# Kernel tuning notes

Measured on AMD Instinct MI355X. Metric: run time of the kernel, lower is better.

The kernel has to match this reference:

```python
import jax, jax.numpy as jnp
import numpy as np

H = 180  # hidden size
T = 240  # timesteps

def lstm_cell_zero_state(x, Wih, bih, bhh):
    # torch nn.LSTMCell called with no (h, c): h = c = 0, so the W_hh term
    # vanishes and f-gate * c_prev vanishes. Gate order in torch: i, f, g, o.
    # x: [B, T, F] -> vectorized over all timesteps at once (no recurrence).
    gates = jnp.einsum('btf,gf->btg', x, Wih) + bih + bhh  # [B, T, 4H]
    i, f, g, o = jnp.split(gates, 4, axis=-1)
    c = jax.nn.sigmoid(i) * jnp.tanh(g)
    h = jax.nn.sigmoid(o) * jnp.tanh(c)
    return h  # [B, T, H]

def setup_inputs() -> dict:
    key = jax.random.key(0)
    ks = jax.random.split(key, 8)
    B = 2048
    s = lambda fan_in: 1.0 / np.sqrt(fan_in)
    x = jax.random.normal(ks[0], (B, 3, 60, T), dtype=jnp.float32)
    # Encoder LSTMCell(180 -> 180)
    W_ih_enc = jax.random.uniform(ks[1], (4 * H, 180), jnp.float32, -s(H), s(H))
    b_ih_enc = jax.random.uniform(ks[2], (4 * H,), jnp.float32, -s(H), s(H))
    b_hh_enc = jax.random.uniform(ks[3], (4 * H,), jnp.float32, -s(H), s(H))
    # Decoder LSTMCell(180 -> 180)
    W_ih_dec = jax.random.uniform(ks[4], (4 * H, H), jnp.float32, -s(H), s(H))
    b_ih_dec = jax.random.uniform(ks[5], (4 * H,), jnp.float32, -s(H), s(H))
    b_hh_dec = jax.random.uniform(ks[6], (4 * H,), jnp.float32, -s(H), s(H))
    # Output Linear(240*180 -> 40)
    W_out = jax.random.uniform(ks[7], (40, T * H), jnp.float32, -s(T * H), s(T * H))
    b_out = jnp.zeros((40,), jnp.float32)
    return {"x": x, "W_ih_enc": W_ih_enc, "b_ih_enc": b_ih_enc, "b_hh_enc": b_hh_enc,
            "W_ih_dec": W_ih_dec, "b_ih_dec": b_ih_dec, "b_hh_dec": b_hh_dec,
            "W_out": W_out, "b_out": b_out}

def reference(x, W_ih_enc, b_ih_enc, b_hh_enc, W_ih_dec, b_ih_dec, b_hh_dec, W_out, b_out):
    B = x.shape[0]
    # Encoder: [B,3,60,240] -> [B,240,3,60] -> [B,240,180]
    xe = jnp.transpose(x, (0, 3, 1, 2)).reshape(B, T, 3 * 60)
    h_enc = lstm_cell_zero_state(xe, W_ih_enc, b_ih_enc, b_hh_enc)  # [B,T,H]
    enc = jax.nn.softmax(h_enc, axis=2)
    # Decoder LSTM (also zero-state every step)
    h_dec = lstm_cell_zero_state(enc, W_ih_dec, b_ih_dec, b_hh_dec)  # [B,T,H]
    flat = h_dec.reshape(B, T * H)
    logits = flat @ W_out.T + b_out  # [B,40]
    out = jax.nn.softmax(logits.reshape(B, 4, 10), axis=2)
    return out
```

## Files before the change

### kernel.cpp

```cpp
#include <hip/hip_runtime.h>
#include <hip/hip_bf16.h>

#define HH 180
#define TT 240
#define KP 192
#define MP 576
#define LSTR 194
#define KOUT 43200
#define BB 2048

typedef __attribute__((ext_vector_type(8))) short short8;
typedef __attribute__((ext_vector_type(4))) float float4v;

__device__ inline unsigned short f2bf(float f) {
    unsigned u = __builtin_bit_cast(unsigned, f);
    u += 0x7fffu + ((u >> 16) & 1u);
    return (unsigned short)(u >> 16);
}
__device__ inline float bf2f(unsigned short h) {
    unsigned u = ((unsigned)h) << 16;
    return __builtin_bit_cast(float, u);
}
__device__ inline float sigm(float x) {
    return __builtin_amdgcn_rcpf(1.f + __expf(-x));
}
__device__ inline float tanh_(float x) {
    return 2.f * __builtin_amdgcn_rcpf(1.f + __expf(-2.f * x)) - 1.f;
}

__global__ void prep_kernel(const float* __restrict__ W1, const float* __restrict__ bi1,
                            const float* __restrict__ bh1, const float* __restrict__ W2,
                            const float* __restrict__ bi2, const float* __restrict__ bh2,
                            const float* __restrict__ Wo,
                            unsigned short* __restrict__ W1p, unsigned short* __restrict__ W2p,
                            float* __restrict__ bEp, float* __restrict__ bDp,
                            unsigned short* __restrict__ Wop, float* __restrict__ logits)
{
    int id = blockIdx.x * 256 + threadIdx.x;
    if (id < MP * KP) {
        int mp = id / KP, k = id % KP;
        int g = mp / KP, h = mp % KP;
        unsigned short v1 = 0, v2 = 0;
        if (h < HH && k < HH) {
            int r = (g == 0) ? h : (g == 1 ? 360 + h : 540 + h);
            v1 = f2bf(W1[r * HH + k]);
            v2 = f2bf(W2[r * HH + k]);
        }
        W1p[id] = v1; W2p[id] = v2;
    }
    if (id < MP) {
        int g = id / KP, h = id % KP;
        float v1 = 0.f, v2 = 0.f;
        if (h < HH) {
            int r = (g == 0) ? h : (g == 1 ? 360 + h : 540 + h);
            v1 = bi1[r] + bh1[r];
            v2 = bi2[r] + bh2[r];
        }
        bEp[id] = v1; bDp[id] = v2;
    }
    if (id < 48 * KOUT) {
        int n = id / KOUT, k = id % KOUT;
        Wop[id] = (n < 40) ? f2bf(Wo[n * KOUT + k]) : (unsigned short)0;
    }
    if (id < BB * 40) logits[id] = 0.f;
}

__global__ __launch_bounds__(256, 2) void phaseA_kernel(
    const float* __restrict__ x, const unsigned short* __restrict__ W1p,
    const unsigned short* __restrict__ W2p, const float* __restrict__ bEp,
    const float* __restrict__ bDp, unsigned short* __restrict__ hdec)
{
    __shared__ __align__(16) unsigned short Xs[128 * LSTR];
    __shared__ float bEs[MP], bDs[MP], sred[256];

    const int tid = threadIdx.x;
    const int b = blockIdx.x >> 1;
    const int t0 = (blockIdx.x & 1) * 112;
    const float* xb = x + (size_t)b * HH * TT;

    for (int i = tid; i < MP; i += 256) { bEs[i] = bEp[i]; bDs[i] = bDp[i]; }

    {
        const int c = tid & 127, half = tid >> 7;
        unsigned* lu = (unsigned*)Xs;
        const int cbase = c * (LSTR / 2);
        for (int i = 0; i < 45; ++i) {
            int f = half * 90 + 2 * i;
            float a0 = xb[f * TT + t0 + c];
            float a1 = xb[(f + 1) * TT + t0 + c];
            lu[cbase + (f >> 1)] = (unsigned)f2bf(a0) | ((unsigned)f2bf(a1) << 16);
        }
        if (half == 0) {
            for (int j = 0; j < 7; ++j) lu[cbase + 90 + j] = 0u;
        }
    }
    __syncthreads();

    const int lane = tid & 63, wv = tid >> 6;
    const int ch = wv >> 1, par = wv & 1;
    const int l15 = lane & 15, l4 = lane >> 4;

    short8 Bf[4][6];
    {
        const unsigned* lu = (const unsigned*)Xs;
        for (int nt = 0; nt < 4; ++nt) {
            int col = ch * 64 + nt * 16 + l15;
            int base = col * (LSTR / 2) + l4 * 4;
            #pragma unroll
            for (int ks = 0; ks < 6; ++ks) {
                union { unsigned u[4]; short8 v; } t;
                int idx = base + ks * 16;
                t.u[0] = lu[idx]; t.u[1] = lu[idx + 1];
                t.u[2] = lu[idx + 2]; t.u[3] = lu[idx + 3];
                Bf[nt][ks] = t.v;
            }
        }
    }
    __syncthreads();

    {
        const uint4* W1q = (const uint4*)W1p;
        for (int tri = par; tri < 12; tri += 2) {
            float4v acc[3][4];
            #pragma unroll
            for (int s = 0; s < 3; ++s)
                #pragma unroll
                for (int n = 0; n < 4; ++n) acc[s][n] = (float4v){0.f, 0.f, 0.f, 0.f};
            #pragma unroll
            for (int sec = 0; sec < 3; ++sec) {
                int abase = (sec * KP + tri * 16 + l15) * (KP / 8) + l4;
                #pragma unroll
                for (int ks = 0; ks < 6; ++ks) {
                    union { uint4 q; short8 v; } a;
                    a.q = W1q[abase + ks * 4];
                    #pragma unroll
                    for (int nt = 0; nt < 4; ++nt)
                        acc[sec][nt] = __builtin_amdgcn_mfma_f32_16x16x32_bf16(
                            a.v, Bf[nt][ks], acc[sec][nt], 0, 0, 0);
                }
            }
            unsigned* lw = (unsigned*)Xs;
            const int h0 = tri * 16 + l4 * 4;
            #pragma unroll
            for (int nt = 0; nt < 4; ++nt) {
                int col = ch * 64 + nt * 16 + l15;
                unsigned pk[2];
                #pragma unroll
                for (int e = 0; e < 4; ++e) {
                    int h = h0 + e;
                    float gi = acc[0][nt][e] + bEs[h];
                    float gg = acc[1][nt][e] + bEs[KP + h];
                    float go = acc[2][nt][e] + bEs[2 * KP + h];
                    float cc = sigm(gi) * tanh_(gg);
                    float hv = sigm(go) * tanh_(cc);
                    ((unsigned short*)pk)[e] = f2bf(__expf(hv));
                }
                lw[col * (LSTR / 2) + (h0 >> 1)] = pk[0];
                lw[col * (LSTR / 2) + (h0 >> 1) + 1] = pk[1];
            }
        }
    }
    __syncthreads();

    {
        const int c = tid & 127, half = tid >> 7;
        const unsigned* lu = (const unsigned*)Xs;
        int base = c * (LSTR / 2) + half * 45;
        float s = 0.f;
        for (int j = 0; j < 45; ++j) {
            unsigned u = lu[base + j];
            s += bf2f((unsigned short)u) + bf2f((unsigned short)(u >> 16));
        }
        sred[half * 128 + c] = s;
    }
    __syncthreads();

    {
        const unsigned* lu = (const unsigned*)Xs;
        for (int nt = 0; nt < 4; ++nt) {
            int col = ch * 64 + nt * 16 + l15;
            int base = col * (LSTR / 2) + l4 * 4;
            #pragma unroll
            for (int ks = 0; ks < 6; ++ks) {
                union { unsigned u[4]; short8 v; } t;
                int idx = base + ks * 16;
                t.u[0] = lu[idx]; t.u[1] = lu[idx + 1];
                t.u[2] = lu[idx + 2]; t.u[3] = lu[idx + 3];
                Bf[nt][ks] = t.v;
            }
        }
    }
    float rs[4];
    #pragma unroll
    for (int nt = 0; nt < 4; ++nt) {
        int col = ch * 64 + nt * 16 + l15;
        rs[nt] = __builtin_amdgcn_rcpf(sred[col] + sred[128 + col]);
    }

    {
        const uint4* W2q = (const uint4*)W2p;
        unsigned short* hout = hdec + (size_t)b * TT * HH;
        for (int tri = par; tri < 12; tri += 2) {
            float4v acc[3][4];
            #pragma unroll
            for (int s = 0; s < 3; ++s)
                #pragma unroll
                for (int n = 0; n < 4; ++n) acc[s][n] = (float4v){0.f, 0.f, 0.f, 0.f};
            #pragma unroll
            for (int sec = 0; sec < 3; ++sec) {
                int abase = (sec * KP + tri * 16 + l15) * (KP / 8) + l4;
                #pragma unroll
                for (int ks = 0; ks < 6; ++ks) {
                    union { uint4 q; short8 v; } a;
                    a.q = W2q[abase + ks * 4];
                    #pragma unroll
                    for (int nt = 0; nt < 4; ++nt)
                        acc[sec][nt] = __builtin_amdgcn_mfma_f32_16x16x32_bf16(
                            a.v, Bf[nt][ks], acc[sec][nt], 0, 0, 0);
                }
            }
            const int h0 = tri * 16 + l4 * 4;
            if (h0 < HH) {
                #pragma unroll
                for (int nt = 0; nt < 4; ++nt) {
                    int col = ch * 64 + nt * 16 + l15;
                    unsigned pk[2];
                    #pragma unroll
                    for (int e = 0; e < 4; ++e) {
                        int h = h0 + e;
                        float gi = acc[0][nt][e] * rs[nt] + bDs[h];
                        float gg = acc[1][nt][e] * rs[nt] + bDs[KP + h];
                        float go = acc[2][nt][e] * rs[nt] + bDs[2 * KP + h];
                        float cc = sigm(gi) * tanh_(gg);
                        float hv = sigm(go) * tanh_(cc);
                        ((unsigned short*)pk)[e] = f2bf(hv);
                    }
                    uint2 pv; pv.x = pk[0]; pv.y = pk[1];
                    *(uint2*)(hout + (size_t)(t0 + col) * HH + h0) = pv;
                }
            }
        }
    }
}

__global__ __launch_bounds__(256, 4) void phaseB_kernel(
    const unsigned short* __restrict__ hdec, const unsigned short* __restrict__ Wop,
    float* __restrict__ logits)
{
    const int tid = threadIdx.x;
    const int lane = tid & 63, wv = tid >> 6;
    const int l15 = lane & 15, l4 = lane >> 4;
    const int m0 = blockIdx.x * 64 + wv * 16;
    const int k0 = blockIdx.y * 1440;

    const uint4* Aq = (const uint4*)hdec;
    const uint4* Bq = (const uint4*)Wop;
    const int QK = KOUT / 8;
    int abase = (m0 + l15) * QK + (k0 >> 3) + l4;
    int bbase = l15 * QK + (k0 >> 3) + l4;

    float4v acc[3];
    #pragma unroll
    for (int n = 0; n < 3; ++n) acc[n] = (float4v){0.f, 0.f, 0.f, 0.f};

    #pragma unroll 3
    for (int ks = 0; ks < 45; ++ks) {
        union { uint4 q; short8 v; } a, b0, b1, b2;
        a.q  = Aq[abase + ks * 4];
        b0.q = Bq[bbase + ks * 4];
        b1.q = Bq[bbase + 16 * QK + ks * 4];
        b2.q = Bq[bbase + 32 * QK + ks * 4];
        acc[0] = __builtin_amdgcn_mfma_f32_16x16x32_bf16(a.v, b0.v, acc[0], 0, 0, 0);
        acc[1] = __builtin_amdgcn_mfma_f32_16x16x32_bf16(a.v, b1.v, acc[1], 0, 0, 0);
        acc[2] = __builtin_amdgcn_mfma_f32_16x16x32_bf16(a.v, b2.v, acc[2], 0, 0, 0);
    }

    #pragma unroll
    for (int nt = 0; nt < 3; ++nt) {
        int o = nt * 16 + l15;
        if (o < 40) {
            #pragma unroll
            for (int e = 0; e < 4; ++e) {
                int row = m0 + l4 * 4 + e;
                atomicAdd(&logits[row * 40 + o], acc[nt][e]);
            }
        }
    }
}

__global__ void out_kernel(const float* __restrict__ logits, const float* __restrict__ bout,
                           float* __restrict__ out)
{
    int id = blockIdx.x * 256 + threadIdx.x;
    if (id >= BB * 4) return;
    int b = id >> 2, j = id & 3;
    float v[10], mx = -1e30f;
    #pragma unroll
    for (int d = 0; d < 10; ++d) {
        v[d] = logits[b * 40 + j * 10 + d] + bout[j * 10 + d];
        mx = fmaxf(mx, v[d]);
    }
    float s = 0.f;
    #pragma unroll
    for (int d = 0; d < 10; ++d) { v[d] = __expf(v[d] - mx); s += v[d]; }
    float r = __builtin_amdgcn_rcpf(s);
    #pragma unroll
    for (int d = 0; d < 10; ++d) out[b * 40 + j * 10 + d] = v[d] * r;
}

extern "C" void kernel_launch(void* const* d_in, const int* in_sizes, int n_in,
                              void* d_out, int out_size, void* d_ws, size_t ws_size,
                              hipStream_t stream)
{
    const float* x    = (const float*)d_in[0];
    const float* W1   = (const float*)d_in[1];
    const float* bi1  = (const float*)d_in[2];
    const float* bh1  = (const float*)d_in[3];
    const float* W2   = (const float*)d_in[4];
    const float* bi2  = (const float*)d_in[5];
    const float* bh2  = (const float*)d_in[6];
    const float* Wo   = (const float*)d_in[7];
    const float* bout = (const float*)d_in[8];

    char* ws = (char*)d_ws;
    unsigned short* W1p = (unsigned short*)(ws + 0);
    unsigned short* W2p = (unsigned short*)(ws + 221184);
    float* bEp          = (float*)(ws + 442368);
    float* bDp          = (float*)(ws + 444928);
    unsigned short* Wop = (unsigned short*)(ws + 447488);
    float* logits       = (float*)(ws + 4594688);
    unsigned short* hdec= (unsigned short*)(ws + 4922368);

    prep_kernel<<<(48 * KOUT + 255) / 256, 256, 0, stream>>>(
        W1, bi1, bh1, W2, bi2, bh2, Wo, W1p, W2p, bEp, bDp, Wop, logits);
    phaseA_kernel<<<BB * 2, 256, 0, stream>>>(x, W1p, W2p, bEp, bDp, hdec);
    phaseB_kernel<<<dim3(32, 30), 256, 0, stream>>>(hdec, Wop, logits);
    out_kernel<<<(BB * 4 + 255) / 256, 256, 0, stream>>>(logits, bout, (float*)d_out);
}
```

Measured before the change: 1.058 ms.

## Split phaseA into four 60-column blocks per batch to raise occupancy

Each batch row is now handled by four blocks of 60 timesteps (padded to 64) instead of two overlapping 128-column blocks. Shared memory is halved, launch bounds allow four blocks per CU, and each wave takes three row tiles instead of six. The loads, softmax row sums and output stores are reorganised for the 4-way split. The aim is better latency hiding through higher occupancy. In exchange, each batch now reads the weight matrices from cache twice as often, and the padding columns are computed and then discarded.

```diff
diff --git a/kernel.cpp b/kernel.cpp
--- a/kernel.cpp
+++ b/kernel.cpp
@@ -6,6 +6,7 @@
 #define KP 192
 #define MP 576
 #define LSTR 194
+#define NCOL 60
 #define KOUT 43200
 #define BB 2048
 
@@ -65,46 +66,55 @@
     if (id < BB * 40) logits[id] = 0.f;
 }
 
-__global__ __launch_bounds__(256, 2) void phaseA_kernel(
+__global__ __launch_bounds__(256, 4) void phaseA_kernel(
     const float* __restrict__ x, const unsigned short* __restrict__ W1p,
     const unsigned short* __restrict__ W2p, const float* __restrict__ bEp,
     const float* __restrict__ bDp, unsigned short* __restrict__ hdec)
 {
-    __shared__ __align__(16) unsigned short Xs[128 * LSTR];
+    __shared__ __align__(16) unsigned short Xs[64 * LSTR];
     __shared__ float bEs[MP], bDs[MP], sred[256];
 
     const int tid = threadIdx.x;
-    const int b = blockIdx.x >> 1;
-    const int t0 = (blockIdx.x & 1) * 112;
+    const int b = blockIdx.x >> 2;
+    const int t0 = (blockIdx.x & 3) * NCOL;
     const float* xb = x + (size_t)b * HH * TT;
 
     for (int i = tid; i < MP; i += 256) { bEs[i] = bEp[i]; bDs[i] = bDp[i]; }
 
     {
-        const int c = tid & 127, half = tid >> 7;
+        const int c = tid & 63, q = tid >> 6;
         unsigned* lu = (unsigned*)Xs;
         const int cbase = c * (LSTR / 2);
-        for (int i = 0; i < 45; ++i) {
-            int f = half * 90 + 2 * i;
-            float a0 = xb[f * TT + t0 + c];
-            float a1 = xb[(f + 1) * TT + t0 + c];
-            lu[cbase + (f >> 1)] = (unsigned)f2bf(a0) | ((unsigned)f2bf(a1) << 16);
-        }
-        if (half == 0) {
-            for (int j = 0; j < 7; ++j) lu[cbase + 90 + j] = 0u;
+        if (c < NCOL) {
+            #pragma unroll
+            for (int i = 0; i < 23; ++i) {
+                int p = q + 4 * i;
+                if (p < 90) {
+                    int f = 2 * p;
+                    float a0 = xb[f * TT + t0 + c];
+                    float a1 = xb[(f + 1) * TT + t0 + c];
+                    lu[cbase + p] = (unsigned)f2bf(a0) | ((unsigned)f2bf(a1) << 16);
+                }
+            }
+            if (q == 0) {
+                for (int j = 90; j < 97; ++j) lu[cbase + j] = 0u;
+            }
+        } else {
+            for (int i = q; i < 97; i += 4) lu[cbase + i] = 0u;
         }
     }
     __syncthreads();
 
     const int lane = tid & 63, wv = tid >> 6;
-    const int ch = wv >> 1, par = wv & 1;
+    const int par = wv;
     const int l15 = lane & 15, l4 = lane >> 4;
 
     short8 Bf[4][6];
     {
         const unsigned* lu = (const unsigned*)Xs;
+        #pragma unroll
         for (int nt = 0; nt < 4; ++nt) {
-            int col = ch * 64 + nt * 16 + l15;
+            int col = nt * 16 + l15;
             int base = col * (LSTR / 2) + l4 * 4;
             #pragma unroll
             for (int ks = 0; ks < 6; ++ks) {
@@ -120,7 +130,9 @@
 
     {
         const uint4* W1q = (const uint4*)W1p;
-        for (int tri = par; tri < 12; tri += 2) {
+        #pragma unroll
+        for (int tt_ = 0; tt_ < 3; ++tt_) {
+            const int tri = par + tt_ * 4;
             float4v acc[3][4];
             #pragma unroll
             for (int s = 0; s < 3; ++s)
@@ -143,7 +155,7 @@
             const int h0 = tri * 16 + l4 * 4;
             #pragma unroll
             for (int nt = 0; nt < 4; ++nt) {
-                int col = ch * 64 + nt * 16 + l15;
+                int col = nt * 16 + l15;
                 unsigned pk[2];
                 #pragma unroll
                 for (int e = 0; e < 4; ++e) {
@@ -163,22 +175,24 @@
     __syncthreads();
 
     {
-        const int c = tid & 127, half = tid >> 7;
+        const int c = tid & 63, q = tid >> 6;
         const unsigned* lu = (const unsigned*)Xs;
-        int base = c * (LSTR / 2) + half * 45;
+        const int lo = q * 23, hi = (lo + 23 < 90) ? lo + 23 : 90;
+        int base = c * (LSTR / 2);
         float s = 0.f;
-        for (int j = 0; j < 45; ++j) {
+        for (int j = lo; j < hi; ++j) {
             unsigned u = lu[base + j];
             s += bf2f((unsigned short)u) + bf2f((unsigned short)(u >> 16));
         }
-        sred[half * 128 + c] = s;
+        sred[q * 64 + c] = s;
     }
     __syncthreads();
 
     {
         const unsigned* lu = (const unsigned*)Xs;
+        #pragma unroll
         for (int nt = 0; nt < 4; ++nt) {
-            int col = ch * 64 + nt * 16 + l15;
+            int col = nt * 16 + l15;
             int base = col * (LSTR / 2) + l4 * 4;
             #pragma unroll
             for (int ks = 0; ks < 6; ++ks) {
@@ -193,14 +207,17 @@
     float rs[4];
     #pragma unroll
     for (int nt = 0; nt < 4; ++nt) {
-        int col = ch * 64 + nt * 16 + l15;
-        rs[nt] = __builtin_amdgcn_rcpf(sred[col] + sred[128 + col]);
+        int col = nt * 16 + l15;
+        rs[nt] = __builtin_amdgcn_rcpf(sred[col] + sred[64 + col] +
+                                       sred[128 + col] + sred[192 + col]);
     }
 
     {
         const uint4* W2q = (const uint4*)W2p;
         unsigned short* hout = hdec + (size_t)b * TT * HH;
-        for (int tri = par; tri < 12; tri += 2) {
+        #pragma unroll
+        for (int tt_ = 0; tt_ < 3; ++tt_) {
+            const int tri = par + tt_ * 4;
             float4v acc[3][4];
             #pragma unroll
             for (int s = 0; s < 3; ++s)
@@ -223,20 +240,22 @@
             if (h0 < HH) {
                 #pragma unroll
                 for (int nt = 0; nt < 4; ++nt) {
-                    int col = ch * 64 + nt * 16 + l15;
-                    unsigned pk[2];
-                    #pragma unroll
-                    for (int e = 0; e < 4; ++e) {
-                        int h = h0 + e;
-                        float gi = acc[0][nt][e] * rs[nt] + bDs[h];
-                        float gg = acc[1][nt][e] * rs[nt] + bDs[KP + h];
-                        float go = acc[2][nt][e] * rs[nt] + bDs[2 * KP + h];
-                        float cc = sigm(gi) * tanh_(gg);
-                        float hv = sigm(go) * tanh_(cc);
-                        ((unsigned short*)pk)[e] = f2bf(hv);
+                    int col = nt * 16 + l15;
+                    if (col < NCOL) {
+                        unsigned pk[2];
+                        #pragma unroll
+                        for (int e = 0; e < 4; ++e) {
+                            int h = h0 + e;
+                            float gi = acc[0][nt][e] * rs[nt] + bDs[h];
+                            float gg = acc[1][nt][e] * rs[nt] + bDs[KP + h];
+                            float go = acc[2][nt][e] * rs[nt] + bDs[2 * KP + h];
+                            float cc = sigm(gi) * tanh_(gg);
+                            float hv = sigm(go) * tanh_(cc);
+                            ((unsigned short*)pk)[e] = f2bf(hv);
+                        }
+                        uint2 pv; pv.x = pk[0]; pv.y = pk[1];
+                        *(uint2*)(hout + (size_t)(t0 + col) * HH + h0) = pv;
                     }
-                    uint2 pv; pv.x = pk[0]; pv.y = pk[1];
-                    *(uint2*)(hout + (size_t)(t0 + col) * HH + h0) = pv;
                 }
             }
         }
@@ -333,7 +352,7 @@
 
     prep_kernel<<<(48 * KOUT + 255) / 256, 256, 0, stream>>>(
         W1, bi1, bh1, W2, bi2, bh2, Wo, W1p, W2p, bEp, bDp, Wop, logits);
-    phaseA_kernel<<<BB * 2, 256, 0, stream>>>(x, W1p, W2p, bEp, bDp, hdec);
+    phaseA_kernel<<<BB * 4, 256, 0, stream>>>(x, W1p, W2p, bEp, bDp, hdec);
     phaseB_kernel<<<dim3(32, 30), 256, 0, stream>>>(hdec, Wop, logits);
     out_kernel<<<(BB * 4 + 255) / 256, 256, 0, stream>>>(logits, bout, (float*)d_out);
 }
```

Measured after the change: 2.261 ms. 2.14x slower.
